# Optimization experiments

Hardware: AMD Instinct MI355X
Metric: run time of the kernel (lower is better)

## Reference

```python
import jax, jax.numpy as jnp
import numpy as np

H = 100  # hidden size of both LSTM layers (fixed in the module)

def lstm_layer(x, w_ih, w_hh, b_ih, b_hh):
    # x: [B, T, I]; w_ih: [4H, I]; w_hh: [4H, H]; biases: [4H]
    # PyTorch gate order: input, forget, cell(g), output.
    B, T, _ = x.shape
    xg = jnp.einsum('bti,gi->btg', x, w_ih) + b_ih + b_hh  # [B, T, 4H], input GEMM hoisted out of the scan
    h0 = jnp.zeros((B, H), x.dtype)
    c0 = jnp.zeros((B, H), x.dtype)
    w_hh_t = w_hh.T  # [H, 4H]

    def step(carry, xg_t):
        h, c = carry
        g = xg_t + h @ w_hh_t                # [B, 4H]
        i, f, gg, o = jnp.split(g, 4, axis=-1)
        i = jax.nn.sigmoid(i)
        f = jax.nn.sigmoid(f)
        gg = jnp.tanh(gg)
        o = jax.nn.sigmoid(o)
        c = f * c + i * gg
        h = o * jnp.tanh(c)
        return (h, c), h

    _, hs = jax.lax.scan(step, (h0, c0), jnp.swapaxes(xg, 0, 1))  # hs: [T, B, H]
    return jnp.swapaxes(hs, 0, 1)  # [B, T, H]


def setup_inputs() -> dict:
    key = jax.random.key(0)
    ks = jax.random.split(key, 13)
    B, T, I = 256, 2048, 8
    s = lambda fan: 1.0 / np.sqrt(fan)
    u = lambda k, shape, fan: jax.random.uniform(k, shape, jnp.float32, -s(fan), s(fan))
    return {
        'x': jax.random.normal(ks[0], (B, T, I), jnp.float32),
        'w_ih1': u(ks[1], (4 * H, I), H), 'w_hh1': u(ks[2], (4 * H, H), H),
        'b_ih1': u(ks[3], (4 * H,), H), 'b_hh1': u(ks[4], (4 * H,), H),
        'w_ih2': u(ks[5], (4 * H, H), H), 'w_hh2': u(ks[6], (4 * H, H), H),
        'b_ih2': u(ks[7], (4 * H,), H), 'b_hh2': u(ks[8], (4 * H,), H),
        'fc1_w': u(ks[9], (25, H), H), 'fc1_b': u(ks[10], (25,), H),
        'fc2_w': u(ks[11], (1, 25), 25), 'fc2_b': u(ks[12], (1,), 25),
    }


def reference(x, w_ih1, w_hh1, b_ih1, b_hh1, w_ih2, w_hh2, b_ih2, b_hh2,
              fc1_w, fc1_b, fc2_w, fc2_b):
    # Dropout layers are identity in eval mode.
    h1 = lstm_layer(x, w_ih1, w_hh1, b_ih1, b_hh1)    # [B, T, H]
    h2 = lstm_layer(h1, w_ih2, w_hh2, b_ih2, b_hh2)   # [B, T, H]
    last = h2[:, -1, :]                               # [B, H]
    y = last @ fc1_w.T + fc1_b                        # [B, 25]
    return y @ fc2_w.T + fc2_b                        # [B, 1]
```

## Files before the change

### kernel.cpp

```cpp
#include <hip/hip_runtime.h>

#define BB 256
#define TT 2048
#define HD 100
#define NG 400

typedef _Float16 h2v __attribute__((ext_vector_type(2)));

__device__ __forceinline__ float fdot2u(unsigned a, unsigned b, float c) {
#if __has_builtin(__builtin_amdgcn_fdot2)
    return __builtin_amdgcn_fdot2(__builtin_bit_cast(h2v, a),
                                  __builtin_bit_cast(h2v, b), c, false);
#else
    h2v av = __builtin_bit_cast(h2v, a), bv = __builtin_bit_cast(h2v, b);
    c = fmaf((float)av[0], (float)bv[0], c);
    c = fmaf((float)av[1], (float)bv[1], c);
    return c;
#endif
}
__device__ __forceinline__ unsigned packh2(float a, float b) {
    h2v p; p[0] = (_Float16)a; p[1] = (_Float16)b;
    return __builtin_bit_cast(unsigned, p);
}
__device__ __forceinline__ float sigmoid_f(float x) {
    return 1.0f / (1.0f + __expf(-x));
}
__device__ __forceinline__ float tanh_f(float x) {
    return 1.0f - 2.0f / (__expf(2.0f * x) + 1.0f);
}

__global__ __launch_bounds__(896, 4) void lstm_fused(
    const float* __restrict__ x,
    const float* __restrict__ w_ih1, const float* __restrict__ w_hh1,
    const float* __restrict__ b_ih1, const float* __restrict__ b_hh1,
    const float* __restrict__ w_ih2, const float* __restrict__ w_hh2,
    const float* __restrict__ b_ih2, const float* __restrict__ b_hh2,
    const float* __restrict__ fc1_w, const float* __restrict__ fc1_b,
    const float* __restrict__ fc2_w, const float* __restrict__ fc2_b,
    float* __restrict__ out)
{
    const int b   = blockIdx.x;
    const int tid = threadIdx.x;

    __shared__ __align__(16) unsigned h1p[52];
    __shared__ __align__(16) unsigned h2p[52];
    __shared__ __align__(16) unsigned xb[2][32][4];
    __shared__ float g1[NG];
    __shared__ float g2[NG];
    __shared__ float h2f[HD];
    __shared__ float fca[25];

    const bool isG1 = (tid < NG);
    const int  g2i  = tid - 448;
    const bool isG2 = (g2i >= 0 && g2i < NG);
    const bool isLd = (tid >= 400 && tid < 432);
    const bool isU1 = (tid < HD);
    const bool isU2 = (g2i >= 0 && g2i < HD);

    unsigned wa[52], wb[52];
    unsigned wx[4];
    float bias = 0.0f, c = 0.0f;

    if (isG1) {
        const float4* ip = (const float4*)(w_ih1 + (size_t)tid * 8);
        float4 v0 = ip[0], v1 = ip[1];
        wx[0] = packh2(v0.x, v0.y); wx[1] = packh2(v0.z, v0.w);
        wx[2] = packh2(v1.x, v1.y); wx[3] = packh2(v1.z, v1.w);
        const float4* hp = (const float4*)(w_hh1 + (size_t)tid * HD);
        #pragma unroll
        for (int k2 = 0; k2 < 25; ++k2) {
            float4 v = hp[k2];
            wa[2*k2]   = packh2(v.x, v.y);
            wa[2*k2+1] = packh2(v.z, v.w);
        }
        wa[50] = 0u; wa[51] = 0u;
        bias = b_ih1[tid] + b_hh1[tid];
    }
    if (isG2) {
        const float4* ip = (const float4*)(w_ih2 + (size_t)g2i * HD);
        const float4* hp = (const float4*)(w_hh2 + (size_t)g2i * HD);
        #pragma unroll
        for (int k2 = 0; k2 < 25; ++k2) {
            float4 v = ip[k2];
            wa[2*k2]   = packh2(v.x, v.y);
            wa[2*k2+1] = packh2(v.z, v.w);
        }
        #pragma unroll
        for (int k2 = 0; k2 < 25; ++k2) {
            float4 v = hp[k2];
            wb[2*k2]   = packh2(v.x, v.y);
            wb[2*k2+1] = packh2(v.z, v.w);
        }
        wa[50] = wa[51] = wb[50] = wb[51] = 0u;
        bias = b_ih2[g2i] + b_hh2[g2i];
    }

    if (tid < 52) h1p[tid] = 0u;
    else if (tid >= 64 && tid < 116) h2p[tid - 64] = 0u;
    if (isLd) {
        const int s = tid - 400;
        const float4* xp = (const float4*)(x + ((size_t)b * TT + s) * 8);
        float4 a0 = xp[0], a1 = xp[1];
        xb[0][s][0] = packh2(a0.x, a0.y); xb[0][s][1] = packh2(a0.z, a0.w);
        xb[0][s][2] = packh2(a1.x, a1.y); xb[0][s][3] = packh2(a1.z, a1.w);
    }
    __syncthreads();

    float4 pa = {0,0,0,0}, pb = {0,0,0,0};

    #pragma unroll 1
    for (int i = 0; i <= TT; ++i) {
        const bool pf = ((i & 31) == 0) && (i + 32 < TT);
        if (isG1 && i < TT) {
            const unsigned* xq = xb[(i >> 5) & 1][i & 31];
            float a0 = bias, a1 = 0.0f;
            a0 = fdot2u(wx[0], xq[0], a0);
            a1 = fdot2u(wx[1], xq[1], a1);
            a0 = fdot2u(wx[2], xq[2], a0);
            a1 = fdot2u(wx[3], xq[3], a1);
            #pragma unroll
            for (int cI = 0; cI < 13; ++cI) {
                uint4 hv = ((const uint4*)h1p)[cI];
                a0 = fdot2u(wa[4*cI+0], hv.x, a0);
                a1 = fdot2u(wa[4*cI+1], hv.y, a1);
                a0 = fdot2u(wa[4*cI+2], hv.z, a0);
                a1 = fdot2u(wa[4*cI+3], hv.w, a1);
            }
            float acc = a0 + a1;
            g1[tid] = (tid < 200 || tid >= 300) ? sigmoid_f(acc) : tanh_f(acc);
        }
        if (isLd && pf) {
            const float4* xp = (const float4*)(x + ((size_t)b * TT + (i + 32) + (tid - 400)) * 8);
            pa = xp[0]; pb = xp[1];
        }
        if (isG2 && i >= 1) {
            float a0 = bias, a1 = 0.0f;
            #pragma unroll
            for (int cI = 0; cI < 13; ++cI) {
                uint4 hv = ((const uint4*)h1p)[cI];
                a0 = fdot2u(wa[4*cI+0], hv.x, a0);
                a1 = fdot2u(wa[4*cI+1], hv.y, a1);
                a0 = fdot2u(wa[4*cI+2], hv.z, a0);
                a1 = fdot2u(wa[4*cI+3], hv.w, a1);
            }
            #pragma unroll
            for (int cI = 0; cI < 13; ++cI) {
                uint4 hv = ((const uint4*)h2p)[cI];
                a0 = fdot2u(wb[4*cI+0], hv.x, a0);
                a1 = fdot2u(wb[4*cI+1], hv.y, a1);
                a0 = fdot2u(wb[4*cI+2], hv.z, a0);
                a1 = fdot2u(wb[4*cI+3], hv.w, a1);
            }
            float acc = a0 + a1;
            g2[g2i] = (g2i < 200 || g2i >= 300) ? sigmoid_f(acc) : tanh_f(acc);
        }
        __syncthreads();
        if (isU1 && i < TT) {
            float gi = g1[tid], gf = g1[HD + tid], gg = g1[2*HD + tid], go = g1[3*HD + tid];
            c = gf * c + gi * gg;
            float h = go * tanh_f(c);
            reinterpret_cast<_Float16*>(h1p)[tid] = (_Float16)h;
        }
        if (isU2 && i >= 1) {
            float gi = g2[g2i], gf = g2[HD + g2i], gg = g2[2*HD + g2i], go = g2[3*HD + g2i];
            c = gf * c + gi * gg;
            float h = go * tanh_f(c);
            reinterpret_cast<_Float16*>(h2p)[g2i] = (_Float16)h;
            if (i == TT) h2f[g2i] = h;
        }
        if (isLd && pf) {
            const int s  = tid - 400;
            const int nb = ((i >> 5) + 1) & 1;
            xb[nb][s][0] = packh2(pa.x, pa.y); xb[nb][s][1] = packh2(pa.z, pa.w);
            xb[nb][s][2] = packh2(pb.x, pb.y); xb[nb][s][3] = packh2(pb.z, pb.w);
        }
        __syncthreads();
    }

    if (tid < 25) {
        float a = fc1_b[tid];
        const float* wp = fc1_w + tid * HD;
        #pragma unroll
        for (int k = 0; k < HD; ++k) a += h2f[k] * wp[k];
        fca[tid] = a;
    }
    __syncthreads();
    if (tid == 0) {
        float y = fc2_b[0];
        #pragma unroll
        for (int m = 0; m < 25; ++m) y += fca[m] * fc2_w[m];
        out[b] = y;
    }
}

extern "C" void kernel_launch(void* const* d_in, const int* in_sizes, int n_in,
                              void* d_out, int out_size, void* d_ws, size_t ws_size,
                              hipStream_t stream) {
    const float* x     = (const float*)d_in[0];
    const float* w_ih1 = (const float*)d_in[1];
    const float* w_hh1 = (const float*)d_in[2];
    const float* b_ih1 = (const float*)d_in[3];
    const float* b_hh1 = (const float*)d_in[4];
    const float* w_ih2 = (const float*)d_in[5];
    const float* w_hh2 = (const float*)d_in[6];
    const float* b_ih2 = (const float*)d_in[7];
    const float* b_hh2 = (const float*)d_in[8];
    const float* fc1_w = (const float*)d_in[9];
    const float* fc1_b = (const float*)d_in[10];
    const float* fc2_w = (const float*)d_in[11];
    const float* fc2_b = (const float*)d_in[12];
    float* out = (float*)d_out;

    lstm_fused<<<BB, 896, 0, stream>>>(x, w_ih1, w_hh1, b_ih1, b_hh1,
                                       w_ih2, w_hh2, b_ih2, b_hh2,
                                       fc1_w, fc1_b, fc2_w, fc2_b, out);
}
```

Measured before the change: 2.923 ms.

## Batch 16 sequences per block and compute LSTM gates with MFMA

Replaces the one-sequence-per-block dot2 kernel with a kernel that processes 16 batch rows per block, computing gate pre-activations through 16x16x32 f16 MFMA instructions. Weights stay in registers as MFMA B fragments. Layers 1 and 2 now run sequentially within each timestep instead of being skewed by one step. The FC head moves into a separate small kernel that reads the final hidden state from workspace. Only 16 blocks are launched, which trades GPU-wide parallelism for matrix-core throughput, and gate activations are stored as fp16.

Result: slower. 6.239 ms (+113.4%).

```diff
diff --git a/kernel.cpp b/kernel.cpp
--- a/kernel.cpp
+++ b/kernel.cpp
@@ -3,194 +3,286 @@
 #define BB 256
 #define TT 2048
 #define HD 100
-#define NG 400
-
+
+typedef _Float16 f16x8 __attribute__((ext_vector_type(8)));
+typedef float f32x4 __attribute__((ext_vector_type(4)));
 typedef _Float16 h2v __attribute__((ext_vector_type(2)));
 
-__device__ __forceinline__ float fdot2u(unsigned a, unsigned b, float c) {
-#if __has_builtin(__builtin_amdgcn_fdot2)
-    return __builtin_amdgcn_fdot2(__builtin_bit_cast(h2v, a),
-                                  __builtin_bit_cast(h2v, b), c, false);
-#else
-    h2v av = __builtin_bit_cast(h2v, a), bv = __builtin_bit_cast(h2v, b);
-    c = fmaf((float)av[0], (float)bv[0], c);
-    c = fmaf((float)av[1], (float)bv[1], c);
-    return c;
-#endif
-}
+#define A1S 272
+#define A2S 464
+#define GSB 848
+
 __device__ __forceinline__ unsigned packh2(float a, float b) {
     h2v p; p[0] = (_Float16)a; p[1] = (_Float16)b;
     return __builtin_bit_cast(unsigned, p);
 }
-__device__ __forceinline__ float sigmoid_f(float x) {
-    return 1.0f / (1.0f + __expf(-x));
-}
+__device__ __forceinline__ float2 unp(unsigned u) {
+    h2v p = __builtin_bit_cast(h2v, u);
+    return make_float2((float)p[0], (float)p[1]);
+}
+__device__ __forceinline__ float rcp_f(float x) {
+#if __has_builtin(__builtin_amdgcn_rcpf)
+    return __builtin_amdgcn_rcpf(x);
+#else
+    return 1.0f / x;
+#endif
+}
+#define LOG2E 1.4426950408889634f
 __device__ __forceinline__ float tanh_f(float x) {
-    return 1.0f - 2.0f / (__expf(2.0f * x) + 1.0f);
-}
-
-__global__ __launch_bounds__(896, 4) void lstm_fused(
+    return fmaf(2.0f, rcp_f(1.0f + exp2f(-2.0f * LOG2E * x)), -1.0f);
+}
+__device__ __forceinline__ f32x4 mfma16(uint4 a, uint4 b, f32x4 c) {
+    return __builtin_amdgcn_mfma_f32_16x16x32_f16(
+        __builtin_bit_cast(f16x8, a), __builtin_bit_cast(f16x8, b), c, 0, 0, 0);
+}
+
+__global__ __launch_bounds__(512, 2) void lstm_mfma(
     const float* __restrict__ x,
     const float* __restrict__ w_ih1, const float* __restrict__ w_hh1,
     const float* __restrict__ b_ih1, const float* __restrict__ b_hh1,
     const float* __restrict__ w_ih2, const float* __restrict__ w_hh2,
     const float* __restrict__ b_ih2, const float* __restrict__ b_hh2,
-    const float* __restrict__ fc1_w, const float* __restrict__ fc1_b,
-    const float* __restrict__ fc2_w, const float* __restrict__ fc2_b,
-    float* __restrict__ out)
+    float* __restrict__ h2f)
 {
-    const int b   = blockIdx.x;
-    const int tid = threadIdx.x;
-
-    __shared__ __align__(16) unsigned h1p[52];
-    __shared__ __align__(16) unsigned h2p[52];
-    __shared__ __align__(16) unsigned xb[2][32][4];
-    __shared__ float g1[NG];
-    __shared__ float g2[NG];
-    __shared__ float h2f[HD];
-    __shared__ float fca[25];
-
-    const bool isG1 = (tid < NG);
-    const int  g2i  = tid - 448;
-    const bool isG2 = (g2i >= 0 && g2i < NG);
-    const bool isLd = (tid >= 400 && tid < 432);
-    const bool isU1 = (tid < HD);
-    const bool isU2 = (g2i >= 0 && g2i < HD);
-
-    unsigned wa[52], wb[52];
-    unsigned wx[4];
-    float bias = 0.0f, c = 0.0f;
-
-    if (isG1) {
-        const float4* ip = (const float4*)(w_ih1 + (size_t)tid * 8);
-        float4 v0 = ip[0], v1 = ip[1];
-        wx[0] = packh2(v0.x, v0.y); wx[1] = packh2(v0.z, v0.w);
-        wx[2] = packh2(v1.x, v1.y); wx[3] = packh2(v1.z, v1.w);
-        const float4* hp = (const float4*)(w_hh1 + (size_t)tid * HD);
-        #pragma unroll
-        for (int k2 = 0; k2 < 25; ++k2) {
-            float4 v = hp[k2];
-            wa[2*k2]   = packh2(v.x, v.y);
-            wa[2*k2+1] = packh2(v.z, v.w);
-        }
-        wa[50] = 0u; wa[51] = 0u;
-        bias = b_ih1[tid] + b_hh1[tid];
-    }
-    if (isG2) {
-        const float4* ip = (const float4*)(w_ih2 + (size_t)g2i * HD);
-        const float4* hp = (const float4*)(w_hh2 + (size_t)g2i * HD);
-        #pragma unroll
-        for (int k2 = 0; k2 < 25; ++k2) {
-            float4 v = ip[k2];
-            wa[2*k2]   = packh2(v.x, v.y);
-            wa[2*k2+1] = packh2(v.z, v.w);
-        }
-        #pragma unroll
-        for (int k2 = 0; k2 < 25; ++k2) {
-            float4 v = hp[k2];
-            wb[2*k2]   = packh2(v.x, v.y);
-            wb[2*k2+1] = packh2(v.z, v.w);
-        }
-        wa[50] = wa[51] = wb[50] = wb[51] = 0u;
-        bias = b_ih2[g2i] + b_hh2[g2i];
-    }
-
-    if (tid < 52) h1p[tid] = 0u;
-    else if (tid >= 64 && tid < 116) h2p[tid - 64] = 0u;
-    if (isLd) {
-        const int s = tid - 400;
-        const float4* xp = (const float4*)(x + ((size_t)b * TT + s) * 8);
-        float4 a0 = xp[0], a1 = xp[1];
-        xb[0][s][0] = packh2(a0.x, a0.y); xb[0][s][1] = packh2(a0.z, a0.w);
-        xb[0][s][2] = packh2(a1.x, a1.y); xb[0][s][3] = packh2(a1.z, a1.w);
+    const int tid  = threadIdx.x;
+    const int lane = tid & 63;
+    const int w    = tid >> 6;
+    const int b0   = blockIdx.x * 16;
+
+    __shared__ __align__(16) _Float16 A1[16 * (A1S / 2)];
+    __shared__ __align__(16) _Float16 A2[16 * (A2S / 2)];
+    __shared__ __align__(16) unsigned G1[16 * (GSB / 4)];
+    __shared__ __align__(16) unsigned G2[16 * (GSB / 4)];
+    __shared__ unsigned XC[2][16][16][4];
+
+    const int col = lane & 15, kg = lane >> 4;
+    const int a1base = col * A1S + kg * 16;
+    const int a2base = col * A2S + kg * 16;
+    const int growb  = (kg * 4) * GSB;
+
+    const int T1 = 3 + (w == 5);
+    const int T2 = 3 + (w == 4);
+
+    uint4 b1[4][4];
+    uint4 b2[4][7];
+    float bias1v[4], am1[4], sc1[4], ad1[4]; int goff1[4];
+    float bias2v[4], am2[4], sc2[4], ad2[4]; int goff2[4];
+
+    #pragma unroll
+    for (int ti = 0; ti < 4; ++ti) {
+        if (ti < T1) {
+            const int nn = (ti < 3) ? (ti * 8 + w) : 24;
+            const int gate = nn * 16 + col;
+            #pragma unroll
+            for (int kt = 0; kt < 4; ++kt) {
+                unsigned q[4];
+                #pragma unroll
+                for (int qq = 0; qq < 4; ++qq) {
+                    const int ka = kt * 32 + kg * 8 + 2 * qq;
+                    const int kb = ka + 1;
+                    float va = (ka < 8) ? w_ih1[gate * 8 + ka]
+                             : (ka < 108 ? w_hh1[(size_t)gate * HD + ka - 8] : 0.f);
+                    float vb = (kb < 8) ? w_ih1[gate * 8 + kb]
+                             : (kb < 108 ? w_hh1[(size_t)gate * HD + kb - 8] : 0.f);
+                    q[qq] = packh2(va, vb);
+                }
+                b1[ti][kt] = make_uint4(q[0], q[1], q[2], q[3]);
+            }
+            bias1v[ti] = b_ih1[gate] + b_hh1[gate];
+            const bool tg = (gate >= 200) && (gate < 300);
+            am1[ti] = tg ? 2.f : 1.f;
+            sc1[ti] = tg ? (-2.f * LOG2E) : (-LOG2E);
+            ad1[ti] = tg ? -1.f : 0.f;
+            const int type = gate / 100, u = gate - type * 100;
+            goff1[ti] = (type * 52 + (u >> 1)) * 4 + (u & 1) * 2;
+        }
+        if (ti < T2) {
+            const int nn = (ti < 3) ? (ti * 8 + w) : 24;
+            const int gate = nn * 16 + col;
+            #pragma unroll
+            for (int kt = 0; kt < 7; ++kt) {
+                unsigned q[4];
+                #pragma unroll
+                for (int qq = 0; qq < 4; ++qq) {
+                    const int ka = kt * 32 + kg * 8 + 2 * qq;
+                    const int kb = ka + 1;
+                    float va = (ka < 100) ? w_ih2[(size_t)gate * HD + ka]
+                             : (ka < 200 ? w_hh2[(size_t)gate * HD + ka - 100] : 0.f);
+                    float vb = (kb < 100) ? w_ih2[(size_t)gate * HD + kb]
+                             : (kb < 200 ? w_hh2[(size_t)gate * HD + kb - 100] : 0.f);
+                    q[qq] = packh2(va, vb);
+                }
+                b2[ti][kt] = make_uint4(q[0], q[1], q[2], q[3]);
+            }
+            bias2v[ti] = b_ih2[gate] + b_hh2[gate];
+            const bool tg = (gate >= 200) && (gate < 300);
+            am2[ti] = tg ? 2.f : 1.f;
+            sc2[ti] = tg ? (-2.f * LOG2E) : (-LOG2E);
+            ad2[ti] = tg ? -1.f : 0.f;
+            const int type = gate / 100, u = gate - type * 100;
+            goff2[ti] = (type * 52 + (u >> 1)) * 4 + (u & 1) * 2;
+        }
+    }
+
+    const bool isUpd = tid < 208;
+    const int  urow = tid & 15;
+    const int  ub   = (tid >> 4) * 8;
+    const int  gub  = urow * GSB + (ub >> 1) * 4;
+    float c1a[8] = {0,0,0,0,0,0,0,0};
+    float c2a[8] = {0,0,0,0,0,0,0,0};
+
+    for (int i = tid; i < 16 * (A1S / 4); i += 512) ((unsigned*)A1)[i] = 0u;
+    for (int i = tid; i < 16 * (A2S / 4); i += 512) ((unsigned*)A2)[i] = 0u;
+    for (int i = tid; i < 16 * (GSB / 4); i += 512) { G1[i] = 0u; G2[i] = 0u; }
+    {
+        const int s = (tid >> 5) & 15, xr = (tid >> 1) & 15, hq = tid & 1;
+        float4 v = *(const float4*)(x + ((size_t)(b0 + xr) * TT + s) * 8 + hq * 4);
+        XC[0][s][xr][hq * 2]     = packh2(v.x, v.y);
+        XC[0][s][xr][hq * 2 + 1] = packh2(v.z, v.w);
     }
     __syncthreads();
-
-    float4 pa = {0,0,0,0}, pb = {0,0,0,0};
+    if (tid < 64) {
+        const int xr = tid >> 2, q = tid & 3;
+        *(unsigned*)((char*)A1 + xr * A1S + q * 4) = XC[0][0][xr][q];
+    }
+    __syncthreads();
 
     #pragma unroll 1
-    for (int i = 0; i <= TT; ++i) {
-        const bool pf = ((i & 31) == 0) && (i + 32 < TT);
-        if (isG1 && i < TT) {
-            const unsigned* xq = xb[(i >> 5) & 1][i & 31];
-            float a0 = bias, a1 = 0.0f;
-            a0 = fdot2u(wx[0], xq[0], a0);
-            a1 = fdot2u(wx[1], xq[1], a1);
-            a0 = fdot2u(wx[2], xq[2], a0);
-            a1 = fdot2u(wx[3], xq[3], a1);
-            #pragma unroll
-            for (int cI = 0; cI < 13; ++cI) {
-                uint4 hv = ((const uint4*)h1p)[cI];
-                a0 = fdot2u(wa[4*cI+0], hv.x, a0);
-                a1 = fdot2u(wa[4*cI+1], hv.y, a1);
-                a0 = fdot2u(wa[4*cI+2], hv.z, a0);
-                a1 = fdot2u(wa[4*cI+3], hv.w, a1);
-            }
-            float acc = a0 + a1;
-            g1[tid] = (tid < 200 || tid >= 300) ? sigmoid_f(acc) : tanh_f(acc);
-        }
-        if (isLd && pf) {
-            const float4* xp = (const float4*)(x + ((size_t)b * TT + (i + 32) + (tid - 400)) * 8);
-            pa = xp[0]; pb = xp[1];
-        }
-        if (isG2 && i >= 1) {
-            float a0 = bias, a1 = 0.0f;
-            #pragma unroll
-            for (int cI = 0; cI < 13; ++cI) {
-                uint4 hv = ((const uint4*)h1p)[cI];
-                a0 = fdot2u(wa[4*cI+0], hv.x, a0);
-                a1 = fdot2u(wa[4*cI+1], hv.y, a1);
-                a0 = fdot2u(wa[4*cI+2], hv.z, a0);
-                a1 = fdot2u(wa[4*cI+3], hv.w, a1);
-            }
-            #pragma unroll
-            for (int cI = 0; cI < 13; ++cI) {
-                uint4 hv = ((const uint4*)h2p)[cI];
-                a0 = fdot2u(wb[4*cI+0], hv.x, a0);
-                a1 = fdot2u(wb[4*cI+1], hv.y, a1);
-                a0 = fdot2u(wb[4*cI+2], hv.z, a0);
-                a1 = fdot2u(wb[4*cI+3], hv.w, a1);
-            }
-            float acc = a0 + a1;
-            g2[g2i] = (g2i < 200 || g2i >= 300) ? sigmoid_f(acc) : tanh_f(acc);
+    for (int t = 0; t < TT; ++t) {
+        float4 xpf = {0.f, 0.f, 0.f, 0.f};
+        const bool dopf = ((t & 15) == 14) && (t + 2 < TT);
+        const int  pfc  = (t + 2) >> 4;
+        const int  pfs = (tid >> 5) & 15, pfr = (tid >> 1) & 15, pfh = tid & 1;
+        if (dopf)
+            xpf = *(const float4*)(x + ((size_t)(b0 + pfr) * TT + (pfc * 16 + pfs)) * 8 + pfh * 4);
+
+        uint4 a1f[4];
+        #pragma unroll
+        for (int kt = 0; kt < 4; ++kt)
+            a1f[kt] = *(const uint4*)((const char*)A1 + a1base + kt * 64);
+        #pragma unroll
+        for (int ti = 0; ti < 4; ++ti) if (ti < T1) {
+            f32x4 acc = {0.f, 0.f, 0.f, 0.f};
+            #pragma unroll
+            for (int kt = 0; kt < 4; ++kt) acc = mfma16(a1f[kt], b1[ti][kt], acc);
+            #pragma unroll
+            for (int j = 0; j < 4; ++j) {
+                float v = acc[j] + bias1v[ti];
+                float a = fmaf(am1[ti], rcp_f(1.f + exp2f(sc1[ti] * v)), ad1[ti]);
+                *(_Float16*)((char*)G1 + growb + j * GSB + goff1[ti]) = (_Float16)a;
+            }
         }
         __syncthreads();
-        if (isU1 && i < TT) {
-            float gi = g1[tid], gf = g1[HD + tid], gg = g1[2*HD + tid], go = g1[3*HD + tid];
-            c = gf * c + gi * gg;
-            float h = go * tanh_f(c);
-            reinterpret_cast<_Float16*>(h1p)[tid] = (_Float16)h;
-        }
-        if (isU2 && i >= 1) {
-            float gi = g2[g2i], gf = g2[HD + g2i], gg = g2[2*HD + g2i], go = g2[3*HD + g2i];
-            c = gf * c + gi * gg;
-            float h = go * tanh_f(c);
-            reinterpret_cast<_Float16*>(h2p)[g2i] = (_Float16)h;
-            if (i == TT) h2f[g2i] = h;
-        }
-        if (isLd && pf) {
-            const int s  = tid - 400;
-            const int nb = ((i >> 5) + 1) & 1;
-            xb[nb][s][0] = packh2(pa.x, pa.y); xb[nb][s][1] = packh2(pa.z, pa.w);
-            xb[nb][s][2] = packh2(pb.x, pb.y); xb[nb][s][3] = packh2(pb.z, pb.w);
+
+        if (isUpd) {
+            const char* gp = (const char*)G1 + gub;
+            uint4 pi = *(const uint4*)(gp);
+            uint4 pf = *(const uint4*)(gp + 208);
+            uint4 pg = *(const uint4*)(gp + 416);
+            uint4 po = *(const uint4*)(gp + 624);
+            unsigned ai[4] = {pi.x, pi.y, pi.z, pi.w};
+            unsigned af[4] = {pf.x, pf.y, pf.z, pf.w};
+            unsigned ag[4] = {pg.x, pg.y, pg.z, pg.w};
+            unsigned ao[4] = {po.x, po.y, po.z, po.w};
+            #pragma unroll
+            for (int q = 0; q < 4; ++q) {
+                const int u0 = ub + 2 * q;
+                float2 vi = unp(ai[q]), vf = unp(af[q]), vg = unp(ag[q]), vo = unp(ao[q]);
+                c1a[2*q]   = vf.x * c1a[2*q]   + vi.x * vg.x;
+                c1a[2*q+1] = vf.y * c1a[2*q+1] + vi.y * vg.y;
+                float h0 = vo.x * tanh_f(c1a[2*q]);
+                float h1 = vo.y * tanh_f(c1a[2*q+1]);
+                if (u0 < 100) {
+                    unsigned hp = packh2(h0, h1);
+                    *(unsigned*)((char*)A1 + urow * A1S + 16 + u0 * 2) = hp;
+                    *(unsigned*)((char*)A2 + urow * A2S + u0 * 2)      = hp;
+                }
+            }
+        }
+        if (dopf) {
+            XC[pfc & 1][pfs][pfr][pfh * 2]     = packh2(xpf.x, xpf.y);
+            XC[pfc & 1][pfs][pfr][pfh * 2 + 1] = packh2(xpf.z, xpf.w);
+        }
+        {
+            const int nt = t + 1;
+            if (nt < TT && tid < 64) {
+                const int xr = tid >> 2, q = tid & 3;
+                *(unsigned*)((char*)A1 + xr * A1S + q * 4) = XC[(nt >> 4) & 1][nt & 15][xr][q];
+            }
         }
         __syncthreads();
-    }
-
-    if (tid < 25) {
-        float a = fc1_b[tid];
-        const float* wp = fc1_w + tid * HD;
-        #pragma unroll
-        for (int k = 0; k < HD; ++k) a += h2f[k] * wp[k];
-        fca[tid] = a;
-    }
-    __syncthreads();
-    if (tid == 0) {
-        float y = fc2_b[0];
-        #pragma unroll
-        for (int m = 0; m < 25; ++m) y += fca[m] * fc2_w[m];
-        out[b] = y;
-    }
+
+        uint4 a2f[7];
+        #pragma unroll
+        for (int kt = 0; kt < 7; ++kt)
+            a2f[kt] = *(const uint4*)((const char*)A2 + a2base + kt * 64);
+        #pragma unroll
+        for (int ti = 0; ti < 4; ++ti) if (ti < T2) {
+            f32x4 acc = {0.f, 0.f, 0.f, 0.f};
+            #pragma unroll
+            for (int kt = 0; kt < 7; ++kt) acc = mfma16(a2f[kt], b2[ti][kt], acc);
+            #pragma unroll
+            for (int j = 0; j < 4; ++j) {
+                float v = acc[j] + bias2v[ti];
+                float a = fmaf(am2[ti], rcp_f(1.f + exp2f(sc2[ti] * v)), ad2[ti]);
+                *(_Float16*)((char*)G2 + growb + j * GSB + goff2[ti]) = (_Float16)a;
+            }
+        }
+        __syncthreads();
+
+        if (isUpd) {
+            const char* gp = (const char*)G2 + gub;
+            uint4 pi = *(const uint4*)(gp);
+            uint4 pf = *(const uint4*)(gp + 208);
+            uint4 pg = *(const uint4*)(gp + 416);
+            uint4 po = *(const uint4*)(gp + 624);
+            unsigned ai[4] = {pi.x, pi.y, pi.z, pi.w};
+            unsigned af[4] = {pf.x, pf.y, pf.z, pf.w};
+            unsigned ag[4] = {pg.x, pg.y, pg.z, pg.w};
+            unsigned ao[4] = {po.x, po.y, po.z, po.w};
+            #pragma unroll
+            for (int q = 0; q < 4; ++q) {
+                const int u0 = ub + 2 * q;
+                float2 vi = unp(ai[q]), vf = unp(af[q]), vg = unp(ag[q]), vo = unp(ao[q]);
+                c2a[2*q]   = vf.x * c2a[2*q]   + vi.x * vg.x;
+                c2a[2*q+1] = vf.y * c2a[2*q+1] + vi.y * vg.y;
+                float h0 = vo.x * tanh_f(c2a[2*q]);
+                float h1 = vo.y * tanh_f(c2a[2*q+1]);
+                if (u0 < 100) {
+                    *(unsigned*)((char*)A2 + urow * A2S + 200 + u0 * 2) = packh2(h0, h1);
+                    if (t == TT - 1) {
+                        h2f[(size_t)(b0 + urow) * HD + u0]     = h0;
+                        h2f[(size_t)(b0 + urow) * HD + u0 + 1] = h1;
+                    }
+                }
+            }
+        }
+    }
+}
+
+__global__ void fc_head(const float* __restrict__ h2,
+                        const float* __restrict__ fc1_w, const float* __restrict__ fc1_b,
+                        const float* __restrict__ fc2_w, const float* __restrict__ fc2_b,
+                        float* __restrict__ out)
+{
+    const int bidx = threadIdx.x;
+    const float* h = h2 + (size_t)bidx * HD;
+    float hv[HD];
+    #pragma unroll
+    for (int kk = 0; kk < HD / 4; ++kk) {
+        float4 v = *(const float4*)(h + 4 * kk);
+        hv[4*kk+0] = v.x; hv[4*kk+1] = v.y; hv[4*kk+2] = v.z; hv[4*kk+3] = v.w;
+    }
+    float y = fc2_b[0];
+    #pragma unroll
+    for (int m = 0; m < 25; ++m) {
+        float a = fc1_b[m];
+        const float* wp = fc1_w + m * HD;
+        #pragma unroll
+        for (int k = 0; k < HD; ++k) a += hv[k] * wp[k];
+        y += a * fc2_w[m];
+    }
+    out[bidx] = y;
 }
 
 extern "C" void kernel_launch(void* const* d_in, const int* in_sizes, int n_in,
@@ -211,7 +303,9 @@
     const float* fc2_b = (const float*)d_in[12];
     float* out = (float*)d_out;
 
-    lstm_fused<<<BB, 896, 0, stream>>>(x, w_ih1, w_hh1, b_ih1, b_hh1,
-                                       w_ih2, w_hh2, b_ih2, b_hh2,
-                                       fc1_w, fc1_b, fc2_w, fc2_b, out);
-}
+    float* h2f = (float*)d_ws;
+
+    lstm_mfma<<<16, 512, 0, stream>>>(x, w_ih1, w_hh1, b_ih1, b_hh1,
+                                      w_ih2, w_hh2, b_ih2, b_hh2, h2f);
+    fc_head<<<1, 256, 0, stream>>>(h2f, fc1_w, fc1_b, fc2_w, fc2_b, out);
+}
```
